# Optimization experiments

Hardware: AMD Instinct MI355X
Metric: run time of the kernel (lower is better)

## Reference

```python
import jax, jax.numpy as jnp
import numpy as np

TEMP = 0.5
NUM_QUERIES = 256
NUM_NEGATIVES = 256
STRONG_THRESHOLD = 0.97


def _l2norm(x):
    n = jnp.sqrt(jnp.sum(x * x, axis=-1, keepdims=True))
    return x / jnp.maximum(n, 1e-12)


def _mls(mu0, mu1, s0, s1, w0, w1):
    # mutual likelihood score, mean over feature dim
    mu0 = _l2norm(mu0)
    mu1 = _l2norm(mu1)
    up = (mu0 * w0 - mu1 * w1) ** 2
    down = s0 * w0 + s1 * w1
    return -0.5 * jnp.mean(up / down + jnp.log(down), axis=-1)


def setup_inputs() -> dict:
    key = jax.random.key(0)
    B, C, H, W, S = 4, 32, 256, 256, 8
    ks = jax.random.split(key, 6)
    weights = jax.random.uniform(ks[0], (B, C, H, W), jnp.float32, 0.1, 1.0)
    mu = jax.random.normal(ks[1], (B, C, H, W), jnp.float32)
    sigma = jax.random.uniform(ks[2], (B, C, H, W), jnp.float32, 0.1, 1.0)
    cls = jax.random.randint(ks[3], (B, H, W), 0, S)
    label = jax.nn.one_hot(cls, S, axis=1, dtype=jnp.float32)  # [B,S,H,W]
    mask = (jax.random.uniform(ks[4], (B, 1, H, W)) < 0.7).astype(jnp.float32)
    prob = jax.random.uniform(ks[5], (B, S, H, W), jnp.float32)
    return {"weights": weights, "mu": mu, "sigma": sigma, "label": label, "mask": mask, "prob": prob}


def _rank_table(m, N):
    # m: bool [S, N]. table[s, r] = pixel index with rank r within class s.
    S = m.shape[0]
    ranks = jnp.cumsum(m, axis=1) - 1
    idx = jnp.where(m, ranks, N)  # out-of-range entries are dropped
    tbl = jnp.zeros((S, N), jnp.int32)
    rows = jnp.broadcast_to(jnp.arange(S)[:, None], (S, N))
    vals = jnp.broadcast_to(jnp.arange(N, dtype=jnp.int32)[None, :], (S, N))
    return tbl.at[rows, idx].set(vals, mode="drop")


def _forward(weights, mu, sigma, label, mask, prob):
    B, C, H, W = mu.shape
    S = label.shape[1]
    N = B * H * W
    Q, NEG = NUM_QUERIES, NUM_NEGATIVES
    mu_f = jnp.transpose(mu, (0, 2, 3, 1)).reshape(N, C)
    sig_f = jnp.transpose(sigma, (0, 2, 3, 1)).reshape(N, C)
    w_f = jnp.transpose(weights, (0, 2, 3, 1)).reshape(N, C)
    valid = jnp.transpose(label * mask, (1, 0, 2, 3)).reshape(S, N)  # [S,N]
    prob_f = jnp.transpose(prob, (1, 0, 2, 3)).reshape(S, N)
    vmask = valid > 0
    hmask = vmask & (prob_f < STRONG_THRESHOLD)
    count = jnp.sum(vmask, axis=1)
    hcount = jnp.sum(hmask, axis=1)
    # prototypes: masked sums over valid pixels (no_grad in original)
    inv_sig_w = w_f / sig_f
    proto_sigma = 1.0 / (valid @ inv_sig_w)                    # [S,C]
    proto_mu = proto_sigma * (valid @ (inv_sig_w * mu_f))      # [S,C]
    proto_weight = 1.0 / (valid @ (1.0 / w_f))                 # [S,C]
    proto_mu, proto_sigma, proto_weight = map(jax.lax.stop_gradient, (proto_mu, proto_sigma, proto_weight))
    tbl_valid = _rank_table(vmask, N)
    tbl_hard = _rank_table(hmask, N)
    keys = jax.random.split(jax.random.key(42), S)

    def per_class(i, key):
        k1, k2, k3 = jax.random.split(key, 3)
        # anchor sampling from hard pixels of class i (differentiable gather)
        ra = jnp.minimum((jax.random.uniform(k1, (Q,)) * hcount[i]).astype(jnp.int32), jnp.maximum(hcount[i] - 1, 0))
        apix = tbl_hard[i, ra]
        a_mu, a_sig, a_w = mu_f[apix], sig_f[apix], w_f[apix]
        # negative class distribution from prototype similarity
        order = (i + 1 + jnp.arange(S - 1)) % S
        sim = _mls(proto_mu[i][None], proto_mu[order], proto_sigma[i][None], proto_sigma[order], proto_weight[i][None], proto_weight[order])
        sim = jnp.where(count[order] > 0, sim, -jnp.inf)
        cls_pick = jax.random.categorical(k2, sim / TEMP, shape=(Q, NEG))
        neg_cls = order[cls_pick]                              # [Q,NEG]
        cnt = count[neg_cls]
        rn = jnp.minimum((jax.random.uniform(k3, (Q, NEG)) * cnt).astype(jnp.int32), jnp.maximum(cnt - 1, 0))
        npix = tbl_valid[neg_cls, rn]                          # [Q,NEG]
        n_mu = jax.lax.stop_gradient(mu_f[npix])
        n_sig = jax.lax.stop_gradient(sig_f[npix])
        n_w = jax.lax.stop_gradient(w_f[npix])
        pos_mu = jnp.broadcast_to(proto_mu[i], (Q, 1, C))
        pos_sig = jnp.broadcast_to(proto_sigma[i], (Q, 1, C))
        pos_w = jnp.broadcast_to(proto_weight[i], (Q, 1, C))
        all_mu = jnp.concatenate([pos_mu, n_mu], axis=1)       # [Q,1+NEG,C]
        all_sig = jnp.concatenate([pos_sig, n_sig], axis=1)
        all_w = jnp.concatenate([pos_w, n_w], axis=1)
        logits = _mls(a_mu[:, None], all_mu, a_sig[:, None], all_sig, a_w[:, None], all_w) / TEMP
        ce = jnp.mean(jax.nn.logsumexp(logits, axis=1) - logits[:, 0])
        ok = (hcount[i] > 0) & (count[i] > 0)
        return jnp.where(ok, ce, 0.0)

    losses = jax.vmap(per_class)(jnp.arange(S), keys)
    valid_num = jnp.sum(count > 0)
    return jnp.sum(losses) / valid_num.astype(losses.dtype)


def reference(weights, mu, sigma, label, mask, prob):
    return _forward(weights, mu, sigma, label, mask, prob)
```

## Files before the change

### kernel.cpp

```cpp
#include <hip/hip_runtime.h>
#include <hip/hip_fp16.h>
#include <stdint.h>


#define NPIX  262144
#define NCLS  8
#define NQ    256
#define NNEG  256
#define NBLK  1024

typedef unsigned short u16;
typedef unsigned int   u32;

struct TFKeys { u32 k1[8][2], k2[8][2], k3[8][2]; };

__host__ __device__ inline void tf2x32(u32 k0, u32 k1, u32 x0, u32 x1, u32& o0, u32& o1) {
  u32 ks2 = k0 ^ k1 ^ 0x1BD11BDAu;
  x0 += k0; x1 += k1;
#define TFR(R) { x0 += x1; x1 = (x1 << (R)) | (x1 >> (32 - (R))); x1 ^= x0; }
  TFR(13) TFR(15) TFR(26) TFR(6)
  x0 += k1;  x1 += ks2 + 1u;
  TFR(17) TFR(29) TFR(16) TFR(24)
  x0 += ks2; x1 += k0 + 2u;
  TFR(13) TFR(15) TFR(26) TFR(6)
  x0 += k0;  x1 += k1 + 3u;
  TFR(17) TFR(29) TFR(16) TFR(24)
  x0 += k1;  x1 += ks2 + 4u;
  TFR(13) TFR(15) TFR(26) TFR(6)
  x0 += ks2; x1 += k0 + 5u;
#undef TFR
  o0 = x0; o1 = x1;
}

__device__ inline float bfv(u16 v) { return __uint_as_float(((u32)v) << 16); }
__device__ inline float lo16(u32 v) { return __uint_as_float(v << 16); }
__device__ inline float hi16(u32 v) { return __uint_as_float(v & 0xFFFF0000u); }
__device__ inline float u01(u32 bits) { return __uint_as_float((bits >> 9) | 0x3F800000u) - 1.0f; }
__device__ inline u32 rbits(u32 k0, u32 k1, u32 idx) { u32 a, b; tf2x32(k0, k1, 0u, idx, a, b); return a ^ b; }
__device__ inline u32 packPQ(float p, float q) {
  return (u32)__half_as_ushort(__float2half(p)) | ((u32)__half_as_ushort(__float2half(q)) << 16);
}
__device__ inline float2 unpackPQ(u32 v) {
  return make_float2(__half2float(__ushort_as_half((u16)(v & 0xFFFFu))),
                     __half2float(__ushort_as_half((u16)(v >> 16))));
}
__device__ inline float frcp(float x) { return __builtin_amdgcn_rcpf(x); }

__global__ __launch_bounds__(256) void k_flags(const u16* __restrict__ lab, const u16* __restrict__ msk,
                                               const u16* __restrict__ prb, unsigned char* __restrict__ flags,
                                               int* __restrict__ blockCnt,
                                               float* __restrict__ protoAcc, float* __restrict__ ceAcc,
                                               int* __restrict__ diag) {
  __shared__ int cnt[16];
  int tid = threadIdx.x;
  if (blockIdx.x == 0) {
    for (int i = tid; i < 768; i += 256) protoAcc[i] = 0.f;
    if (tid < 8) ceAcc[tid] = 0.f;
    if (tid == 0) diag[0] = 0;
  }
  if (tid < 16) cnt[tid] = 0;
  __syncthreads();
  int n = blockIdx.x * 256 + tid;
  int b = n >> 16, hw = n & 65535;
  float m = bfv(msk[(b << 16) + hw]);
  int cls = 0; bool v = false;
  for (int s = 0; s < 8; s++) {
    float l = bfv(lab[((size_t)(b * 8 + s) << 16) + hw]);
    if (l * m > 0.f) { cls = s; v = true; }
  }
  bool h = false;
  if (v) { float p = bfv(prb[((size_t)(b * 8 + cls) << 16) + hw]); h = p < 0.97f; }
  flags[n] = (unsigned char)(cls | (v ? 16 : 0) | (h ? 32 : 0));
  if (v) atomicAdd(&cnt[cls], 1);
  if (h) atomicAdd(&cnt[8 + cls], 1);
  __syncthreads();
  if (tid < 16) blockCnt[tid * NBLK + blockIdx.x] = cnt[tid];
}

__global__ __launch_bounds__(256) void k_pq_proto(const u16* __restrict__ mu, const u16* __restrict__ wgt,
                                                  const u16* __restrict__ sig,
                                                  const unsigned char* __restrict__ flags,
                                                  u32* __restrict__ PQ, float* __restrict__ protoAcc) {
  __shared__ u32 tile[256 * 33];
  __shared__ float pacc[4 * 808];
  int t = threadIdx.x;
  for (int i = t; i < 4 * 808; i += 256) pacc[i] = 0.f;
  __syncthreads();
  int n0 = blockIdx.x * 512;
  int b = n0 >> 16;
  int hwt = (n0 & 65535) + 2 * t;
  size_t cb = ((size_t)(b * 32)) << 16;
  u32 f2 = *(const u16*)(flags + n0 + 2 * t);
  int cls0 = (int)(f2 & 7u);         bool v0 = (f2 & 16u) != 0u;
  int cls1 = (int)((f2 >> 8) & 7u);  bool v1 = ((f2 >> 8) & 16u) != 0u;
  int copy = (t & 3) * 808;
  int base0 = copy + cls0 * 100, base1 = copy + cls1 * 100;
  u32 m2[32];
  float ss0 = 0.f, ss1 = 0.f;
  #pragma unroll
  for (int c = 0; c < 32; c++) {
    m2[c] = *(const u32*)(mu + cb + ((size_t)c << 16) + hwt);
    float a = lo16(m2[c]), d = hi16(m2[c]);
    ss0 += a * a; ss1 += d * d;
  }
  float rn0 = 1.0f / fmaxf(sqrtf(ss0), 1e-12f);
  float rn1 = 1.0f / fmaxf(sqrtf(ss1), 1e-12f);
  u32 pk0[32], pk1[32];
  #pragma unroll
  for (int c = 0; c < 32; c++) {
    u32 w2 = *(const u32*)(wgt + cb + ((size_t)c << 16) + hwt);
    u32 s2 = *(const u32*)(sig + cb + ((size_t)c << 16) + hwt);
    float wl = lo16(w2), wh = hi16(w2);
    float sl = lo16(s2), sh = hi16(s2);
    float ml = lo16(m2[c]), mh = hi16(m2[c]);
    pk0[c] = packPQ(ml * rn0 * wl, sl * wl);
    pk1[c] = packPQ(mh * rn1 * wh, sh * wh);
    if (v0) {
      float isw = wl / sl;
      atomicAdd(&pacc[base0 + c * 3 + 0], isw);
      atomicAdd(&pacc[base0 + c * 3 + 1], isw * ml);
      atomicAdd(&pacc[base0 + c * 3 + 2], 1.0f / wl);
    }
    if (v1) {
      float isw = wh / sh;
      atomicAdd(&pacc[base1 + c * 3 + 0], isw);
      atomicAdd(&pacc[base1 + c * 3 + 1], isw * mh);
      atomicAdd(&pacc[base1 + c * 3 + 2], 1.0f / wh);
    }
  }
  #pragma unroll
  for (int ch = 0; ch < 2; ch++) {
    if ((t >> 7) == ch) {
      int l = t & 127;
      #pragma unroll
      for (int c = 0; c < 32; c++) {
        tile[(2 * l + 0) * 33 + c] = pk0[c];
        tile[(2 * l + 1) * 33 + c] = pk1[c];
      }
    }
    __syncthreads();
    uint4* dst = (uint4*)(PQ + (size_t)(n0 + ch * 256) * 32);
    for (int k = t; k < 2048; k += 256) {
      int p = k >> 3, c4 = (k & 7) * 4;
      dst[k] = make_uint4(tile[p * 33 + c4], tile[p * 33 + c4 + 1],
                          tile[p * 33 + c4 + 2], tile[p * 33 + c4 + 3]);
    }
    __syncthreads();
  }
  for (int idx = t; idx < 800; idx += 256) {
    int c8 = idx / 100, rem = idx - c8 * 100;
    if (rem < 96) {
      float sum = pacc[idx] + pacc[idx + 808] + pacc[idx + 1616] + pacc[idx + 2424];
      atomicAdd(&protoAcc[c8 * 96 + rem], sum);
    }
  }
}

__global__ __launch_bounds__(256) void k_place(const unsigned char* __restrict__ flags,
                                               const int* __restrict__ blockCnt,
                                               int* __restrict__ tblV, int* __restrict__ tblH,
                                               int* __restrict__ counts) {
  __shared__ int wcnt[4][16];
  __shared__ int sOff[16], sTot[16];
  int tid = threadIdx.x;
  int blk = blockIdx.x;
  if (tid < 16) { sOff[tid] = 0; sTot[tid] = 0; }
  __syncthreads();
  {
    int ctr = tid & 15, seg = tid >> 4;
    const int* row = blockCnt + ctr * NBLK + seg * 64;
    int lim = blk - seg * 64;
    int pre = 0, tot = 0;
    #pragma unroll 8
    for (int l = 0; l < 64; ++l) {
      int v = row[l];
      tot += v;
      pre += (l < lim) ? v : 0;
    }
    atomicAdd(&sOff[ctr], pre);
    if (blk == 0) atomicAdd(&sTot[ctr], tot);
  }
  __syncthreads();
  if (blk == 0 && tid < 16) counts[tid] = sTot[tid];
  int n = blk * 256 + tid;
  int f = flags[n];
  int cls = f & 15; bool v = (f & 16) != 0, h = (f & 32) != 0;
  int wave = tid >> 6, lane = tid & 63;
  unsigned long long below = (1ull << lane) - 1ull;
  int rv = 0, rh = 0;
  for (int s = 0; s < 8; s++) {
    unsigned long long bv = __ballot(v && (cls == s));
    unsigned long long bh = __ballot(h && (cls == s));
    if (lane == 0) { wcnt[wave][s] = __popcll(bv); wcnt[wave][8 + s] = __popcll(bh); }
    if (cls == s) { rv = __popcll(bv & below); rh = __popcll(bh & below); }
  }
  __syncthreads();
  int preV = 0, preH = 0;
  for (int w2 = 0; w2 < wave; w2++) { preV += wcnt[w2][cls]; preH += wcnt[w2][8 + cls]; }
  if (v) tblV[(size_t)cls * NPIX + sOff[cls] + preV + rv] = n;
  if (h) tblH[(size_t)cls * NPIX + sOff[8 + cls] + preH + rh] = n;
}

__global__ void k_protoFinal(const float* __restrict__ protoAcc, const int* __restrict__ counts,
                             u32* __restrict__ protoPQ, float* __restrict__ simL,
                             int* __restrict__ diag) {
  __shared__ float sP[256], sQ[256];
  __shared__ int alive;
  int tid = threadIdx.x;
  if (tid == 0) alive = 0;
  float a0 = protoAcc[tid * 3 + 0], a1 = protoAcc[tid * 3 + 1], a2 = protoAcc[tid * 3 + 2];
  bool have = counts[tid >> 5] > 0;
  bool ok = (a0 > 0.f) && (a2 > 0.f);
  __syncthreads();
  if (have && !ok) atomicOr(diag, 2);
  if (have && ok) alive = 1;
  float psig = 1.0f / a0;
  float pmu  = psig * a1;
  float pw   = 1.0f / a2;
  float sq = (have && ok) ? pmu * pmu : 0.f;
  #pragma unroll
  for (int d = 1; d < 32; d <<= 1) sq += __shfl_xor(sq, d);
  float rn = 1.0f / fmaxf(sqrtf(sq), 1e-12f);
  float pP = (have && ok) ? pmu * rn * pw : 0.f;
  float pQ = (have && ok) ? psig * pw : 0.f;
  sP[tid] = pP; sQ[tid] = pQ;
  protoPQ[tid] = packPQ(pP, pQ);
  __syncthreads();
  if (tid == 0 && alive == 0) atomicOr(diag, 32);
  if (tid < 64) {
    int i = tid >> 3, j = tid & 7;
    if (j < 7) {
      int o = (i + 1 + j) & 7;
      float acc = 0.f;
      for (int c = 0; c < 32; c++) {
        float d = sP[i * 32 + c] - sP[o * 32 + c];
        float dn = sQ[i * 32 + c] + sQ[o * 32 + c];
        acc += d * d / dn + logf(dn);
      }
      float sim = -0.5f * (acc * (1.0f / 32.0f));
      simL[i * 8 + j] = (counts[o] > 0) ? (sim * 2.0f) : -INFINITY;
    }
  }
}

__global__ __launch_bounds__(256) void k_sample(TFKeys K, const float* __restrict__ simL,
                                                const int* __restrict__ counts,
                                                const int* __restrict__ tblV, const int* __restrict__ tblH,
                                                const u32* __restrict__ PQ, const u32* __restrict__ protoPQ,
                                                float* __restrict__ ceAcc, int* __restrict__ diag) {
  __shared__ float redM[4], redS[4];
  int blk = blockIdx.x;
  int i = blk >> 8, q = blk & 255;
  int t = threadIdx.x;
  u32 abits = rbits(K.k1[i][0], K.k1[i][1], (u32)q);
  float au = u01(abits);
  int hc = counts[8 + i];
  int ra = (int)(au * (float)hc);
  int cap = hc - 1; if (cap < 0) cap = 0;
  if (ra > cap) ra = cap; if (ra < 0) ra = 0;
  int ap = tblH[(size_t)i * NPIX + ra];
  if (ap < 0) ap = 0; if (ap > NPIX - 1) ap = NPIX - 1;
  const uint4* A4 = (const uint4*)(PQ + (size_t)ap * 32);
  u32 rem = (u32)(q * 256 + t);
  u32 k20 = K.k2[i][0], k21 = K.k2[i][1];
  float Lr[7];
  #pragma unroll
  for (int j = 0; j < 7; j++) Lr[j] = simL[i * 8 + j];
  float mg = 0.f; int pick = 0;
  #pragma unroll
  for (int j = 0; j < 7; j++) {
    u32 bits = rbits(k20, k21, rem * 7u + (u32)j);
    float f = u01(bits);
    float u = fmaxf(f, 1.17549435e-38f);
    float g = -__logf(-__logf(u));
    float v = g + Lr[j];
    if (j == 0) { mg = v; } else if (v > mg) { mg = v; pick = j; }
  }
  int nc = (i + 1 + pick) & 7;
  u32 bits3 = rbits(K.k3[i][0], K.k3[i][1], rem);
  float u3 = u01(bits3);
  int cntv = counts[nc];
  int rn = (int)(u3 * (float)cntv);
  int cap2 = cntv - 1; if (cap2 < 0) cap2 = 0;
  if (rn > cap2) rn = cap2; if (rn < 0) rn = 0;
  int np = tblV[(size_t)nc * NPIX + rn];
  if (np < 0) np = 0; if (np > NPIX - 1) np = NPIX - 1;
  const uint4* B = (const uint4*)(PQ + (size_t)np * 32);
  float accN = 0.f;
  #pragma unroll
  for (int k = 0; k < 8; k++) {
    uint4 ua = A4[k], ub = B[k];
    float2 fa, fb; float d, dn;
    fa = unpackPQ(ua.x); fb = unpackPQ(ub.x); d = fa.x - fb.x; dn = fa.y + fb.y; accN += d * d * frcp(dn) + __logf(dn);
    fa = unpackPQ(ua.y); fb = unpackPQ(ub.y); d = fa.x - fb.x; dn = fa.y + fb.y; accN += d * d * frcp(dn) + __logf(dn);
    fa = unpackPQ(ua.z); fb = unpackPQ(ub.z); d = fa.x - fb.x; dn = fa.y + fb.y; accN += d * d * frcp(dn) + __logf(dn);
    fa = unpackPQ(ua.w); fb = unpackPQ(ub.w); d = fa.x - fb.x; dn = fa.y + fb.y; accN += d * d * frcp(dn) + __logf(dn);
  }
  float lN = -(accN * (1.0f / 32.0f));
  float l0 = 0.f;
  if (t == 0) {
    const uint4* B0 = (const uint4*)(protoPQ + i * 32);
    float acc0 = 0.f;
    #pragma unroll
    for (int k = 0; k < 8; k++) {
      uint4 ua = A4[k], ub = B0[k];
      float2 fa, fb; float d, dn;
      fa = unpackPQ(ua.x); fb = unpackPQ(ub.x); d = fa.x - fb.x; dn = fa.y + fb.y; acc0 += d * d * frcp(dn) + __logf(dn);
      fa = unpackPQ(ua.y); fb = unpackPQ(ub.y); d = fa.x - fb.x; dn = fa.y + fb.y; acc0 += d * d * frcp(dn) + __logf(dn);
      fa = unpackPQ(ua.z); fb = unpackPQ(ub.z); d = fa.x - fb.x; dn = fa.y + fb.y; acc0 += d * d * frcp(dn) + __logf(dn);
      fa = unpackPQ(ua.w); fb = unpackPQ(ub.w); d = fa.x - fb.x; dn = fa.y + fb.y; acc0 += d * d * frcp(dn) + __logf(dn);
    }
    l0 = -(acc0 * (1.0f / 32.0f));
  }
  bool bad = !(lN == lN) || (t == 0 && !(l0 == l0));
  if (__ballot(bad) != 0ull && (t & 63) == 0) atomicOr(diag, 8);
  float lm = (t == 0) ? fmaxf(lN, l0) : lN;
  #pragma unroll
  for (int d = 1; d < 64; d <<= 1) lm = fmaxf(lm, __shfl_xor(lm, d));
  if ((t & 63) == 0) redM[t >> 6] = lm;
  __syncthreads();
  float M = fmaxf(fmaxf(redM[0], redM[1]), fmaxf(redM[2], redM[3]));
  float es = __expf(lN - M) + ((t == 0) ? __expf(l0 - M) : 0.f);
  #pragma unroll
  for (int d = 1; d < 64; d <<= 1) es += __shfl_xor(es, d);
  if ((t & 63) == 0) redS[t >> 6] = es;
  __syncthreads();
  if (t == 0) {
    float S = redS[0] + redS[1] + redS[2] + redS[3];
    float ce = (M + __logf(S)) - l0;
    atomicAdd(&ceAcc[i], ce);
  }
}

__global__ void k_final(const float* __restrict__ ceAcc, const int* __restrict__ counts,
                        const int* __restrict__ diag, u32* __restrict__ out) {
  if (blockIdx.x == 0 && threadIdx.x == 0) {
    float loss = 0.f; int vn = 0;
    int db = diag[0];
    for (int i = 0; i < 8; i++) {
      if (counts[i] > 0) vn++;
      float ce = ceAcc[i];
      if (counts[i] > 0 && counts[8 + i] > 0) {
        if (!(ce == ce)) db |= 4;
        loss += ce * (1.0f / 256.0f);
      }
    }
    if (vn == 0) db |= 1;
    loss = loss / (float)vn;
    if (!(loss == loss) && db == 0) db = 16;
    if (db != 0) loss = 4096.0f * (float)(1 + db);
    u32 fb = __float_as_uint(loss);
    u32 bv = (fb + 0x7FFFu + ((fb >> 16) & 1u)) >> 16;
    out[0] = (fb & 0xFFFF0000u) | (bv & 0xFFFFu);
  }
}

extern "C" void kernel_launch(void* const* d_in, const int* in_sizes, int n_in,
                              void* d_out, int out_size, void* d_ws, size_t ws_size,
                              hipStream_t stream) {
  (void)in_sizes; (void)n_in; (void)out_size; (void)ws_size;
  const u16* wgt = (const u16*)d_in[0];
  const u16* mu  = (const u16*)d_in[1];
  const u16* sig = (const u16*)d_in[2];
  const u16* lab = (const u16*)d_in[3];
  const u16* msk = (const u16*)d_in[4];
  const u16* prb = (const u16*)d_in[5];

  char* wp = (char*)d_ws;
  auto take = [&](size_t bytes) -> void* { void* p = (void*)wp; wp += ((bytes + 255) & ~(size_t)255); return p; };
  u32*   PQ       = (u32*)  take((size_t)NPIX * 32 * 4);
  int*   tblV     = (int*)  take((size_t)NCLS * NPIX * 4);
  int*   tblH     = (int*)  take((size_t)NCLS * NPIX * 4);
  unsigned char* flags = (unsigned char*)take(NPIX);
  int*   blockCnt = (int*)  take(16 * NBLK * 4);
  float* protoAcc = (float*)take(768 * 4);
  u32*   protoPQ  = (u32*)  take(256 * 4);
  float* simL     = (float*)take(64 * 4);
  int*   counts   = (int*)  take(16 * 4);
  float* ceAcc    = (float*)take(8 * 4);
  int*   diag     = (int*)  take(4);

  TFKeys K;
  for (u32 i = 0; i < 8; i++) {
    u32 ki0, ki1;
    tf2x32(0u, 42u, 0u, i, ki0, ki1);
    tf2x32(ki0, ki1, 0u, 0u, K.k1[i][0], K.k1[i][1]);
    tf2x32(ki0, ki1, 0u, 1u, K.k2[i][0], K.k2[i][1]);
    tf2x32(ki0, ki1, 0u, 2u, K.k3[i][0], K.k3[i][1]);
  }

  k_flags<<<1024, 256, 0, stream>>>(lab, msk, prb, flags, blockCnt, protoAcc, ceAcc, diag);
  k_pq_proto<<<512, 256, 0, stream>>>(mu, wgt, sig, flags, PQ, protoAcc);
  k_place<<<1024, 256, 0, stream>>>(flags, blockCnt, tblV, tblH, counts);
  k_protoFinal<<<1, 256, 0, stream>>>(protoAcc, counts, protoPQ, simL, diag);
  k_sample<<<2048, 256, 0, stream>>>(K, simL, counts, tblV, tblH, PQ, protoPQ, ceAcc, diag);
  k_final<<<1, 64, 0, stream>>>(ceAcc, counts, diag, (u32*)d_out);
}
```

Baseline: 225.6 us.

## Fuse flag computation into PQ kernel and fold tiny kernels into neighbors

Flag and count computation moves from its own kernel into k_pq_proto, with each thread handling its two pixels and writing per-half-block counts. The single-block prototype finalisation moves into block 0 of k_place. The final reduction moves into the last k_sample block through a completion counter. Accumulator zeroing becomes a memset. This removes three launches and one pass over the flags inputs. The cost is serialized prototype work at the tail of k_place block 0 and a last-block atomic/fence pattern in k_sample.

```diff
diff --git a/kernel.cpp b/kernel.cpp
--- a/kernel.cpp
+++ b/kernel.cpp
@@ -46,53 +46,45 @@
 }
 __device__ inline float frcp(float x) { return __builtin_amdgcn_rcpf(x); }
 
-__global__ __launch_bounds__(256) void k_flags(const u16* __restrict__ lab, const u16* __restrict__ msk,
-                                               const u16* __restrict__ prb, unsigned char* __restrict__ flags,
-                                               int* __restrict__ blockCnt,
-                                               float* __restrict__ protoAcc, float* __restrict__ ceAcc,
-                                               int* __restrict__ diag) {
-  __shared__ int cnt[16];
-  int tid = threadIdx.x;
-  if (blockIdx.x == 0) {
-    for (int i = tid; i < 768; i += 256) protoAcc[i] = 0.f;
-    if (tid < 8) ceAcc[tid] = 0.f;
-    if (tid == 0) diag[0] = 0;
-  }
-  if (tid < 16) cnt[tid] = 0;
-  __syncthreads();
-  int n = blockIdx.x * 256 + tid;
-  int b = n >> 16, hw = n & 65535;
-  float m = bfv(msk[(b << 16) + hw]);
-  int cls = 0; bool v = false;
-  for (int s = 0; s < 8; s++) {
-    float l = bfv(lab[((size_t)(b * 8 + s) << 16) + hw]);
-    if (l * m > 0.f) { cls = s; v = true; }
-  }
-  bool h = false;
-  if (v) { float p = bfv(prb[((size_t)(b * 8 + cls) << 16) + hw]); h = p < 0.97f; }
-  flags[n] = (unsigned char)(cls | (v ? 16 : 0) | (h ? 32 : 0));
-  if (v) atomicAdd(&cnt[cls], 1);
-  if (h) atomicAdd(&cnt[8 + cls], 1);
-  __syncthreads();
-  if (tid < 16) blockCnt[tid * NBLK + blockIdx.x] = cnt[tid];
-}
-
 __global__ __launch_bounds__(256) void k_pq_proto(const u16* __restrict__ mu, const u16* __restrict__ wgt,
                                                   const u16* __restrict__ sig,
-                                                  const unsigned char* __restrict__ flags,
+                                                  const u16* __restrict__ lab, const u16* __restrict__ msk,
+                                                  const u16* __restrict__ prb,
+                                                  unsigned char* __restrict__ flags,
+                                                  int* __restrict__ blockCnt,
                                                   u32* __restrict__ PQ, float* __restrict__ protoAcc) {
   __shared__ u32 tile[256 * 33];
   __shared__ float pacc[4 * 808];
+  __shared__ int cnt[32];
   int t = threadIdx.x;
   for (int i = t; i < 4 * 808; i += 256) pacc[i] = 0.f;
+  if (t < 32) cnt[t] = 0;
   __syncthreads();
   int n0 = blockIdx.x * 512;
   int b = n0 >> 16;
   int hwt = (n0 & 65535) + 2 * t;
   size_t cb = ((size_t)(b * 32)) << 16;
-  u32 f2 = *(const u16*)(flags + n0 + 2 * t);
-  int cls0 = (int)(f2 & 7u);         bool v0 = (f2 & 16u) != 0u;
-  int cls1 = (int)((f2 >> 8) & 7u);  bool v1 = ((f2 >> 8) & 16u) != 0u;
+  u32 mk2 = *(const u32*)(msk + (((size_t)b) << 16) + hwt);
+  float mk0 = lo16(mk2), mk1 = hi16(mk2);
+  int cls0 = 0, cls1 = 0; bool v0 = false, v1 = false;
+  for (int s = 0; s < 8; s++) {
+    u32 l2 = *(const u32*)(lab + (((size_t)(b * 8 + s)) << 16) + hwt);
+    if (lo16(l2) * mk0 > 0.f) { cls0 = s; v0 = true; }
+    if (hi16(l2) * mk1 > 0.f) { cls1 = s; v1 = true; }
+  }
+  bool h0 = false, h1 = false;
+  if (v0) { float p = bfv(prb[(((size_t)(b * 8 + cls0)) << 16) + hwt]);     h0 = p < 0.97f; }
+  if (v1) { float p = bfv(prb[(((size_t)(b * 8 + cls1)) << 16) + hwt + 1]); h1 = p < 0.97f; }
+  {
+    int half16 = (t >> 7) * 16;
+    if (v0) atomicAdd(&cnt[half16 + cls0], 1);
+    if (h0) atomicAdd(&cnt[half16 + 8 + cls0], 1);
+    if (v1) atomicAdd(&cnt[half16 + cls1], 1);
+    if (h1) atomicAdd(&cnt[half16 + 8 + cls1], 1);
+    u32 f0 = (u32)cls0 | (v0 ? 16u : 0u) | (h0 ? 32u : 0u);
+    u32 f1 = (u32)cls1 | (v1 ? 16u : 0u) | (h1 ? 32u : 0u);
+    *(u16*)(flags + n0 + 2 * t) = (u16)(f0 | (f1 << 8));
+  }
   int copy = (t & 3) * 808;
   int base0 = copy + cls0 * 100, base1 = copy + cls1 * 100;
   u32 m2[32];
@@ -154,14 +146,20 @@
       atomicAdd(&protoAcc[c8 * 96 + rem], sum);
     }
   }
+  if (t < 32) blockCnt[(t & 15) * NBLK + 2 * blockIdx.x + (t >> 4)] = cnt[(t >> 4) * 16 + (t & 15)];
 }
 
 __global__ __launch_bounds__(256) void k_place(const unsigned char* __restrict__ flags,
                                                const int* __restrict__ blockCnt,
                                                int* __restrict__ tblV, int* __restrict__ tblH,
-                                               int* __restrict__ counts) {
+                                               int* __restrict__ counts,
+                                               const float* __restrict__ protoAcc,
+                                               u32* __restrict__ protoPQ, float* __restrict__ simL,
+                                               int* __restrict__ diag) {
   __shared__ int wcnt[4][16];
   __shared__ int sOff[16], sTot[16];
+  __shared__ float sP[256], sQ[256];
+  __shared__ int alive;
   int tid = threadIdx.x;
   int blk = blockIdx.x;
   if (tid < 16) { sOff[tid] = 0; sTot[tid] = 0; }
@@ -199,46 +197,40 @@
   for (int w2 = 0; w2 < wave; w2++) { preV += wcnt[w2][cls]; preH += wcnt[w2][8 + cls]; }
   if (v) tblV[(size_t)cls * NPIX + sOff[cls] + preV + rv] = n;
   if (h) tblH[(size_t)cls * NPIX + sOff[8 + cls] + preH + rh] = n;
-}
-
-__global__ void k_protoFinal(const float* __restrict__ protoAcc, const int* __restrict__ counts,
-                             u32* __restrict__ protoPQ, float* __restrict__ simL,
-                             int* __restrict__ diag) {
-  __shared__ float sP[256], sQ[256];
-  __shared__ int alive;
-  int tid = threadIdx.x;
-  if (tid == 0) alive = 0;
-  float a0 = protoAcc[tid * 3 + 0], a1 = protoAcc[tid * 3 + 1], a2 = protoAcc[tid * 3 + 2];
-  bool have = counts[tid >> 5] > 0;
-  bool ok = (a0 > 0.f) && (a2 > 0.f);
-  __syncthreads();
-  if (have && !ok) atomicOr(diag, 2);
-  if (have && ok) alive = 1;
-  float psig = 1.0f / a0;
-  float pmu  = psig * a1;
-  float pw   = 1.0f / a2;
-  float sq = (have && ok) ? pmu * pmu : 0.f;
-  #pragma unroll
-  for (int d = 1; d < 32; d <<= 1) sq += __shfl_xor(sq, d);
-  float rn = 1.0f / fmaxf(sqrtf(sq), 1e-12f);
-  float pP = (have && ok) ? pmu * rn * pw : 0.f;
-  float pQ = (have && ok) ? psig * pw : 0.f;
-  sP[tid] = pP; sQ[tid] = pQ;
-  protoPQ[tid] = packPQ(pP, pQ);
-  __syncthreads();
-  if (tid == 0 && alive == 0) atomicOr(diag, 32);
-  if (tid < 64) {
-    int i = tid >> 3, j = tid & 7;
-    if (j < 7) {
-      int o = (i + 1 + j) & 7;
-      float acc = 0.f;
-      for (int c = 0; c < 32; c++) {
-        float d = sP[i * 32 + c] - sP[o * 32 + c];
-        float dn = sQ[i * 32 + c] + sQ[o * 32 + c];
-        acc += d * d / dn + logf(dn);
+  if (blk == 0) {
+    if (tid == 0) alive = 0;
+    float a0 = protoAcc[tid * 3 + 0], a1 = protoAcc[tid * 3 + 1], a2 = protoAcc[tid * 3 + 2];
+    bool have = sTot[tid >> 5] > 0;
+    bool ok = (a0 > 0.f) && (a2 > 0.f);
+    __syncthreads();
+    if (have && !ok) atomicOr(diag, 2);
+    if (have && ok) alive = 1;
+    float psig = 1.0f / a0;
+    float pmu  = psig * a1;
+    float pw   = 1.0f / a2;
+    float sq = (have && ok) ? pmu * pmu : 0.f;
+    #pragma unroll
+    for (int d = 1; d < 32; d <<= 1) sq += __shfl_xor(sq, d);
+    float rn = 1.0f / fmaxf(sqrtf(sq), 1e-12f);
+    float pP = (have && ok) ? pmu * rn * pw : 0.f;
+    float pQ = (have && ok) ? psig * pw : 0.f;
+    sP[tid] = pP; sQ[tid] = pQ;
+    protoPQ[tid] = packPQ(pP, pQ);
+    __syncthreads();
+    if (tid == 0 && alive == 0) atomicOr(diag, 32);
+    if (tid < 64) {
+      int i = tid >> 3, j = tid & 7;
+      if (j < 7) {
+        int o = (i + 1 + j) & 7;
+        float acc = 0.f;
+        for (int c = 0; c < 32; c++) {
+          float d = sP[i * 32 + c] - sP[o * 32 + c];
+          float dn = sQ[i * 32 + c] + sQ[o * 32 + c];
+          acc += d * d / dn + logf(dn);
+        }
+        float sim = -0.5f * (acc * (1.0f / 32.0f));
+        simL[i * 8 + j] = (sTot[o] > 0) ? (sim * 2.0f) : -INFINITY;
       }
-      float sim = -0.5f * (acc * (1.0f / 32.0f));
-      simL[i * 8 + j] = (counts[o] > 0) ? (sim * 2.0f) : -INFINITY;
     }
   }
 }
@@ -247,7 +239,8 @@
                                                 const int* __restrict__ counts,
                                                 const int* __restrict__ tblV, const int* __restrict__ tblH,
                                                 const u32* __restrict__ PQ, const u32* __restrict__ protoPQ,
-                                                float* __restrict__ ceAcc, int* __restrict__ diag) {
+                                                float* __restrict__ ceAcc, int* __restrict__ diag,
+                                                int* __restrict__ doneCnt, u32* __restrict__ out) {
   __shared__ float redM[4], redS[4];
   int blk = blockIdx.x;
   int i = blk >> 8, q = blk & 255;
@@ -330,28 +323,29 @@
     float ce = (M + __logf(S)) - l0;
     atomicAdd(&ceAcc[i], ce);
   }
-}
-
-__global__ void k_final(const float* __restrict__ ceAcc, const int* __restrict__ counts,
-                        const int* __restrict__ diag, u32* __restrict__ out) {
-  if (blockIdx.x == 0 && threadIdx.x == 0) {
-    float loss = 0.f; int vn = 0;
-    int db = diag[0];
-    for (int i = 0; i < 8; i++) {
-      if (counts[i] > 0) vn++;
-      float ce = ceAcc[i];
-      if (counts[i] > 0 && counts[8 + i] > 0) {
-        if (!(ce == ce)) db |= 4;
-        loss += ce * (1.0f / 256.0f);
+  __syncthreads();
+  if (t == 0) {
+    __threadfence();
+    u32 done = (u32)atomicAdd(doneCnt, 1);
+    if (done == 2047u) {
+      int db = atomicOr(diag, 0);
+      float loss = 0.f; int vn = 0;
+      for (int ii = 0; ii < 8; ii++) {
+        if (counts[ii] > 0) vn++;
+        float ce = atomicAdd(&ceAcc[ii], 0.0f);
+        if (counts[ii] > 0 && counts[8 + ii] > 0) {
+          if (!(ce == ce)) db |= 4;
+          loss += ce * (1.0f / 256.0f);
+        }
       }
-    }
-    if (vn == 0) db |= 1;
-    loss = loss / (float)vn;
-    if (!(loss == loss) && db == 0) db = 16;
-    if (db != 0) loss = 4096.0f * (float)(1 + db);
-    u32 fb = __float_as_uint(loss);
-    u32 bv = (fb + 0x7FFFu + ((fb >> 16) & 1u)) >> 16;
-    out[0] = (fb & 0xFFFF0000u) | (bv & 0xFFFFu);
+      if (vn == 0) db |= 1;
+      loss = loss / (float)vn;
+      if (!(loss == loss) && db == 0) db = 16;
+      if (db != 0) loss = 4096.0f * (float)(1 + db);
+      u32 fb = __float_as_uint(loss);
+      u32 bv = (fb + 0x7FFFu + ((fb >> 16) & 1u)) >> 16;
+      out[0] = (fb & 0xFFFF0000u) | (bv & 0xFFFFu);
+    }
   }
 }
 
@@ -379,6 +373,8 @@
   int*   counts   = (int*)  take(16 * 4);
   float* ceAcc    = (float*)take(8 * 4);
   int*   diag     = (int*)  take(4);
+  int*   doneCnt  = (int*)  take(4);
+  size_t tailBytes = (size_t)(wp - (char*)protoAcc);
 
   TFKeys K;
   for (u32 i = 0; i < 8; i++) {
@@ -389,10 +385,8 @@
     tf2x32(ki0, ki1, 0u, 2u, K.k3[i][0], K.k3[i][1]);
   }
 
-  k_flags<<<1024, 256, 0, stream>>>(lab, msk, prb, flags, blockCnt, protoAcc, ceAcc, diag);
-  k_pq_proto<<<512, 256, 0, stream>>>(mu, wgt, sig, flags, PQ, protoAcc);
-  k_place<<<1024, 256, 0, stream>>>(flags, blockCnt, tblV, tblH, counts);
-  k_protoFinal<<<1, 256, 0, stream>>>(protoAcc, counts, protoPQ, simL, diag);
-  k_sample<<<2048, 256, 0, stream>>>(K, simL, counts, tblV, tblH, PQ, protoPQ, ceAcc, diag);
-  k_final<<<1, 64, 0, stream>>>(ceAcc, counts, diag, (u32*)d_out);
-}
+  hipMemsetAsync(protoAcc, 0, tailBytes, stream);
+  k_pq_proto<<<512, 256, 0, stream>>>(mu, wgt, sig, lab, msk, prb, flags, blockCnt, PQ, protoAcc);
+  k_place<<<1024, 256, 0, stream>>>(flags, blockCnt, tblV, tblH, counts, protoAcc, protoPQ, simL, diag);
+  k_sample<<<2048, 256, 0, stream>>>(K, simL, counts, tblV, tblH, PQ, protoPQ, ceAcc, diag, doneCnt, (u32*)d_out);
+}
```

After: 251.9 us. 11.7% more time.
